# Optimization experiments

Measured on AMD Instinct MI355X. Metric: run time of the kernel, lower is better.

Reference implementation:

```python
import jax, jax.numpy as jnp
import numpy as np
import math

EMBED_DIM = 1024
NUM_HEADS = 16
D_K = EMBED_DIM // NUM_HEADS  # 64 qubits per head
BATCH, SEQ = 4, 2048


def setup_inputs() -> dict:
    key = jax.random.key(0)
    k_x, k_th, k_w, k_b = jax.random.split(key, 4)
    x = jax.random.normal(k_x, (BATCH, SEQ, EMBED_DIM), dtype=jnp.float32)
    # trainable RX angle per head per qubit (tq.RX has one param each)
    theta = jax.random.normal(k_th, (NUM_HEADS, D_K), dtype=jnp.float32)
    # out_linear
    lim = 1.0 / math.sqrt(EMBED_DIM)
    w_out = jax.random.uniform(k_w, (EMBED_DIM, EMBED_DIM), jnp.float32, -lim, lim)
    b_out = jax.random.uniform(k_b, (EMBED_DIM,), jnp.float32, -lim, lim)
    return {"x": x, "theta": theta, "w_out": w_out, "b_out": b_out}


def reference(x, theta, w_out, b_out):
    B, S, E = x.shape
    H, d_k = theta.shape
    # Quantum head: RX(x_i) then RX(theta_i) on |0>, measure PauliZ ->
    # <Z_i> = cos(x_i + theta_i). No entangling gates in the code path.
    ang = x.reshape(B, S, H, d_k) + theta  # broadcast [H,d_k]
    qkv = jnp.cos(ang).transpose(0, 2, 1, 3)  # [B,H,S,d_k]; Q == K == V
    scale = 1.0 / math.sqrt(d_k)
    scores = jnp.einsum('bhqd,bhkd->bhqk', qkv, qkv) * scale
    attn = jax.nn.softmax(scores, axis=-1)  # dropout is identity in eval
    out = jnp.einsum('bhqk,bhkd->bhqd', attn, qkv)
    out = out.transpose(0, 2, 1, 3).reshape(B, S, E)
    return out @ w_out.T + b_out
```

## Files before the change

kernel.cpp:

```cpp
#include <hip/hip_runtime.h>


#define B_  4
#define S_  2048
#define H_  16
#define D_  64
#define E_  1024
#define EXP2_SCALE 0.18033688011112043f

typedef unsigned short u16;
typedef unsigned int u32;
typedef __attribute__((ext_vector_type(8))) short short8;
typedef __attribute__((ext_vector_type(4))) float floatx4;

static __device__ __forceinline__ float bf2f(u16 v) {
    return __uint_as_float(((unsigned)v) << 16);
}
static __device__ __forceinline__ u16 f2bf(float f) {
    unsigned u = __float_as_uint(f);
    return (u16)((u + 0x7FFFu + ((u >> 16) & 1u)) >> 16);
}
static __device__ __forceinline__ u32 pack_bf16_trunc(float lo, float hi) {
    return __builtin_amdgcn_perm(__float_as_uint(hi), __float_as_uint(lo), 0x07060302u);
}
static __device__ __forceinline__ short8 scale8(short8 v) {
    short8 o;
#pragma unroll
    for (int i = 0; i < 8; i++)
        o[i] = (short)f2bf(bf2f((u16)v[i]) * EXP2_SCALE);
    return o;
}

#define KSWZ(r, c) ((((r)) << 6) + (((c) ^ ((((r)) & 7) << 3))))

__global__ __launch_bounds__(256) void prep_kernel(const float* __restrict__ x,
                                                   const float* __restrict__ theta,
                                                   const float* __restrict__ W,
                                                   u16* __restrict__ qkv,
                                                   u16* __restrict__ qkvT,
                                                   u16* __restrict__ Wb) {
    __shared__ __align__(16) u16 TQ[64][72];
    int blk = blockIdx.x;
    int tid = threadIdx.x;
    if (blk >= 2048) {
        int i = ((blk - 2048) * 256 + tid) * 4;
        float4 w = *(const float4*)(W + i);
        ushort4 o;
        o.x = f2bf(w.x); o.y = f2bf(w.y); o.z = f2bf(w.z); o.w = f2bf(w.w);
        *(ushort4*)(Wb + i) = o;
        return;
    }
    int stile = blk & 31;
    int bh    = blk >> 5;
    int b     = bh >> 4;
    int h     = bh & 15;
    int i     = tid >> 2;
    int d0    = (tid & 3) << 4;
    int s0    = stile << 6;
    int s     = s0 + i;

    const float* xp = x + ((size_t)(b * S_ + s)) * E_ + h * D_ + d0;
    const float* tp = theta + h * D_ + d0;

    u16 ov[16];
#pragma unroll
    for (int j = 0; j < 16; j += 4) {
        float4 xv = *(const float4*)(xp + j);
        float4 tv = *(const float4*)(tp + j);
        ov[j]     = f2bf(__cosf(xv.x + tv.x));
        ov[j + 1] = f2bf(__cosf(xv.y + tv.y));
        ov[j + 2] = f2bf(__cosf(xv.z + tv.z));
        ov[j + 3] = f2bf(__cosf(xv.w + tv.w));
    }

    u16* qp = qkv + ((size_t)bh * S_ + s) * D_ + d0;
    *(uint4*)qp       = *(uint4*)&ov[0];
    *(uint4*)(qp + 8) = *(uint4*)&ov[8];

#pragma unroll
    for (int j = 0; j < 16; j++) TQ[d0 + j][i] = ov[j];
    __syncthreads();

    int d  = tid >> 2;
    int j0 = (tid & 3) << 4;
    u16 tmp[16];
#pragma unroll
    for (int j = 0; j < 16; j++) tmp[j] = TQ[d][j0 + j];
    u16* qtp = qkvT + ((size_t)bh * D_ + d) * S_ + s0 + j0;
    *(uint4*)qtp       = *(uint4*)&tmp[0];
    *(uint4*)(qtp + 8) = *(uint4*)&tmp[8];
}

__global__ __launch_bounds__(256, 4) void attn_kernel(const u16* __restrict__ qkv,
                                                      const u16* __restrict__ qkvT,
                                                      u16* __restrict__ aout) {
    int blk0 = blockIdx.x;
    int blk  = (blk0 & 7) * 128 + (blk0 >> 3);
    int qt   = blk & 15;
    int bh   = blk >> 4;
    int b    = bh >> 4;
    int h    = bh & 15;
    int tid  = threadIdx.x;
    int wave = tid >> 6;
    int lane = tid & 63;
    int lq   = lane & 15;
    int lg   = lane >> 4;
    int r    = tid >> 2;
    int c0   = (tid & 3) << 4;

    __shared__ __align__(16) u16 Kt[64 * 64];
    __shared__ __align__(16) u16 Vt[64 * 64];
    __shared__ __align__(16) u16 Pb[4][32 * 64];

    const u16* base  = qkv  + (size_t)bh * S_ * D_;
    const u16* baseT = qkvT + (size_t)bh * D_ * S_;
    int s0 = qt * 128;

    short8 bq[2][2];
#pragma unroll
    for (int rf = 0; rf < 2; rf++) {
        const u16* qrow = base + (size_t)(s0 + wave * 32 + rf * 16 + lq) * D_ + lg * 8;
        bq[rf][0] = scale8(*(const short8*)qrow);
        bq[rf][1] = scale8(*(const short8*)(qrow + 32));
    }

    floatx4 oacc[2][4] = {{{0,0,0,0},{0,0,0,0},{0,0,0,0},{0,0,0,0}},
                          {{0,0,0,0},{0,0,0,0},{0,0,0,0},{0,0,0,0}}};
    float lsum[2] = {0.f, 0.f};

    {
        const u16* p = base + (size_t)r * D_ + c0;
        *(uint4*)&Kt[KSWZ(r, c0)]     = *(const uint4*)p;
        *(uint4*)&Kt[KSWZ(r, c0 + 8)] = *(const uint4*)(p + 8);
        const u16* p2 = baseT + (size_t)r * S_ + c0;
        *(uint4*)&Vt[KSWZ(r, c0)]     = *(const uint4*)p2;
        *(uint4*)&Vt[KSWZ(r, c0 + 8)] = *(const uint4*)(p2 + 8);
    }
    __syncthreads();

    for (int kt = 0; kt < S_ / 64; kt++) {
#pragma unroll
        for (int t = 0; t < 4; t++) {
            short8 a0 = *(short8*)&Kt[KSWZ(t * 16 + lq, lg * 8)];
            short8 a1 = *(short8*)&Kt[KSWZ(t * 16 + lq, 32 + lg * 8)];
            floatx4 sct[2];
#pragma unroll
            for (int rf = 0; rf < 2; rf++) {
                floatx4 acc = {0, 0, 0, 0};
                acc = __builtin_amdgcn_mfma_f32_16x16x32_bf16(a0, bq[rf][0], acc, 0, 0, 0);
                sct[rf] = __builtin_amdgcn_mfma_f32_16x16x32_bf16(a1, bq[rf][1], acc, 0, 0, 0);
            }
#pragma unroll
            for (int rf = 0; rf < 2; rf++) {
                float p0 = __builtin_amdgcn_exp2f(sct[rf][0]);
                float p1 = __builtin_amdgcn_exp2f(sct[rf][1]);
                float p2 = __builtin_amdgcn_exp2f(sct[rf][2]);
                float p3 = __builtin_amdgcn_exp2f(sct[rf][3]);
                lsum[rf] += (p0 + p1) + (p2 + p3);
                uint2 w;
                w.x = pack_bf16_trunc(p0, p1);
                w.y = pack_bf16_trunc(p2, p3);
                *(uint2*)&Pb[wave][KSWZ(rf * 16 + lq, t * 16 + lg * 4)] = w;
            }
        }

        asm volatile("s_waitcnt lgkmcnt(0)" ::: "memory");

        short8 bp[2][2];
#pragma unroll
        for (int rf = 0; rf < 2; rf++) {
            bp[rf][0] = *(short8*)&Pb[wave][KSWZ(rf * 16 + lq, lg * 8)];
            bp[rf][1] = *(short8*)&Pb[wave][KSWZ(rf * 16 + lq, 32 + lg * 8)];
        }
        __builtin_amdgcn_s_setprio(1);
#pragma unroll
        for (int t = 0; t < 4; t++) {
            short8 av0 = *(short8*)&Vt[KSWZ(t * 16 + lq, lg * 8)];
            short8 av1 = *(short8*)&Vt[KSWZ(t * 16 + lq, 32 + lg * 8)];
#pragma unroll
            for (int rf = 0; rf < 2; rf++) {
                oacc[rf][t] = __builtin_amdgcn_mfma_f32_16x16x32_bf16(av0, bp[rf][0], oacc[rf][t], 0, 0, 0);
                oacc[rf][t] = __builtin_amdgcn_mfma_f32_16x16x32_bf16(av1, bp[rf][1], oacc[rf][t], 0, 0, 0);
            }
        }
        __builtin_amdgcn_s_setprio(0);

        __syncthreads();
        if (kt < S_ / 64 - 1) {
            const u16* p = base + (size_t)((kt + 1) * 64 + r) * D_ + c0;
            uint4 k0 = *(const uint4*)p;
            uint4 k1 = *(const uint4*)(p + 8);
            const u16* p2 = baseT + (size_t)r * S_ + (kt + 1) * 64 + c0;
            uint4 v0 = *(const uint4*)p2;
            uint4 v1 = *(const uint4*)(p2 + 8);
            *(uint4*)&Kt[KSWZ(r, c0)]     = k0;
            *(uint4*)&Kt[KSWZ(r, c0 + 8)] = k1;
            *(uint4*)&Vt[KSWZ(r, c0)]     = v0;
            *(uint4*)&Vt[KSWZ(r, c0 + 8)] = v1;
        }
        __syncthreads();
    }

#pragma unroll
    for (int rf = 0; rf < 2; rf++) {
        lsum[rf] += __shfl_xor(lsum[rf], 16);
        lsum[rf] += __shfl_xor(lsum[rf], 32);
    }
#pragma unroll
    for (int rf = 0; rf < 2; rf++) {
        float inv = 1.0f / fmaxf(lsum[rf], 1e-20f);
        int srow = s0 + wave * 32 + rf * 16 + lq;
        u16* arow = aout + ((size_t)(b * S_ + srow)) * E_ + h * D_;
#pragma unroll
        for (int t = 0; t < 4; t++)
#pragma unroll
            for (int rr = 0; rr < 4; rr++)
                arow[t * 16 + lg * 4 + rr] = f2bf(oacc[rf][t][rr] * inv);
    }
}

__global__ __launch_bounds__(256) void proj_kernel(const u16* __restrict__ A,
                                                   const u16* __restrict__ Wb,
                                                   const float* __restrict__ bias,
                                                   float* __restrict__ out) {
    int m0   = blockIdx.x * 128;
    int n0   = blockIdx.y * 128;
    int tid  = threadIdx.x;
    int wave = tid >> 6;
    int wm   = wave >> 1;
    int wn   = wave & 1;
    int lane = tid & 63;
    int lq   = lane & 15;
    int lg   = lane >> 4;
    int r    = tid >> 1;
    int c0   = (tid & 1) * 32;

    __shared__ __align__(16) u16 As[128][72];
    __shared__ __align__(16) u16 Bs[128][72];

    floatx4 acc[4][4];
#pragma unroll
    for (int i = 0; i < 4; i++)
#pragma unroll
        for (int j = 0; j < 4; j++) acc[i][j] = (floatx4){0, 0, 0, 0};

    for (int kc = 0; kc < E_; kc += 64) {
        __syncthreads();
        const u16* pa = A + (size_t)(m0 + r) * E_ + kc + c0;
        const u16* pw = Wb + (size_t)(n0 + r) * E_ + kc + c0;
#pragma unroll
        for (int j = 0; j < 4; j++) {
            *(uint4*)&As[r][c0 + j * 8] = *(const uint4*)(pa + j * 8);
            *(uint4*)&Bs[r][c0 + j * 8] = *(const uint4*)(pw + j * 8);
        }
        __syncthreads();

#pragma unroll
        for (int c = 0; c < 2; c++) {
            short8 af[4], bf[4];
#pragma unroll
            for (int i = 0; i < 4; i++)
                af[i] = *(short8*)&As[wm * 64 + i * 16 + lq][c * 32 + lg * 8];
#pragma unroll
            for (int j = 0; j < 4; j++)
                bf[j] = *(short8*)&Bs[wn * 64 + j * 16 + lq][c * 32 + lg * 8];
#pragma unroll
            for (int i = 0; i < 4; i++)
#pragma unroll
                for (int j = 0; j < 4; j++)
                    acc[i][j] = __builtin_amdgcn_mfma_f32_16x16x32_bf16(af[i], bf[j], acc[i][j], 0, 0, 0);
        }
    }

#pragma unroll
    for (int j = 0; j < 4; j++) {
        int nidx = n0 + wn * 64 + j * 16 + lq;
        float bv = bias[nidx];
#pragma unroll
        for (int i = 0; i < 4; i++) {
#pragma unroll
            for (int rr = 0; rr < 4; rr++) {
                int row = m0 + wm * 64 + i * 16 + lg * 4 + rr;
                out[(size_t)row * E_ + nidx] = acc[i][j][rr] + bv;
            }
        }
    }
}

extern "C" void kernel_launch(void* const* d_in, const int* in_sizes, int n_in,
                              void* d_out, int out_size, void* d_ws, size_t ws_size,
                              hipStream_t stream) {
    const float* x     = (const float*)d_in[0];
    const float* theta = (const float*)d_in[1];
    const float* w_out = (const float*)d_in[2];
    const float* b_out = (const float*)d_in[3];
    float* out = (float*)d_out;

    char* ws = (char*)d_ws;
    const size_t QKV_BYTES = (size_t)B_ * H_ * S_ * D_ * sizeof(u16);
    u16* qkv  = (u16*)ws;
    u16* qkvT = (u16*)(ws + QKV_BYTES);
    u16* aout = (u16*)(ws + 2 * QKV_BYTES);
    u16* wbf_safe = (u16*)(ws + 3 * QKV_BYTES);

    prep_kernel<<<3072, 256, 0, stream>>>(x, theta, w_out, qkv, qkvT, wbf_safe);
    attn_kernel<<<(B_ * H_) * (S_ / 128), 256, 0, stream>>>(qkv, qkvT, aout);
    dim3 pg(B_ * S_ / 128, E_ / 128);
    proj_kernel<<<pg, 256, 0, stream>>>(aout, wbf_safe, b_out, out);
}
```

Baseline: 196.2 us.

## Keep softmax probabilities in registers and use 16x16x16 MFMA for PV

Drops the per-wave shared-memory staging of the P tile. Each lane's score output layout already matches the B operand of the 16x16x16 bf16 MFMA, so the probabilities feed the PV product straight from registers. This removes the LDS write, the wait and the read-back per key tile. In exchange it issues twice as many smaller MFMAs with narrower V reads, and it frees LDS, which may help occupancy.

New measurement: 204.2 us. 1.04x slower.

```diff
diff --git a/kernel.cpp b/kernel.cpp
--- a/kernel.cpp
+++ b/kernel.cpp
@@ -11,6 +11,7 @@
 typedef unsigned short u16;
 typedef unsigned int u32;
 typedef __attribute__((ext_vector_type(8))) short short8;
+typedef __attribute__((ext_vector_type(4))) short short4v;
 typedef __attribute__((ext_vector_type(4))) float floatx4;
 
 static __device__ __forceinline__ float bf2f(u16 v) {
@@ -29,6 +30,21 @@
     for (int i = 0; i < 8; i++)
         o[i] = (short)f2bf(bf2f((u16)v[i]) * EXP2_SCALE);
     return o;
+}
+
+#if defined(__has_builtin)
+#if __has_builtin(__builtin_amdgcn_mfma_f32_16x16x16bf16_1k)
+#define MFMA16_HAVE_BUILTIN 1
+#endif
+#endif
+static __device__ __forceinline__ floatx4 mfma16(short4v a, short4v b, floatx4 c) {
+#ifdef MFMA16_HAVE_BUILTIN
+    return __builtin_amdgcn_mfma_f32_16x16x16bf16_1k(a, b, c, 0, 0, 0);
+#else
+    floatx4 d = c;
+    asm("v_mfma_f32_16x16x16_bf16 %0, %1, %2, %0" : "+v"(d) : "v"(a), "v"(b));
+    return d;
+#endif
 }
 
 #define KSWZ(r, c) ((((r)) << 6) + (((c) ^ ((((r)) & 7) << 3))))
@@ -110,7 +126,6 @@
 
     __shared__ __align__(16) u16 Kt[64 * 64];
     __shared__ __align__(16) u16 Vt[64 * 64];
-    __shared__ __align__(16) u16 Pb[4][32 * 64];
 
     const u16* base  = qkv  + (size_t)bh * S_ * D_;
     const u16* baseT = qkvT + (size_t)bh * D_ * S_;
@@ -139,6 +154,7 @@
     __syncthreads();
 
     for (int kt = 0; kt < S_ / 64; kt++) {
+        short4v pb[2][4];
 #pragma unroll
         for (int t = 0; t < 4; t++) {
             short8 a0 = *(short8*)&Kt[KSWZ(t * 16 + lq, lg * 8)];
@@ -160,27 +176,18 @@
                 uint2 w;
                 w.x = pack_bf16_trunc(p0, p1);
                 w.y = pack_bf16_trunc(p2, p3);
-                *(uint2*)&Pb[wave][KSWZ(rf * 16 + lq, t * 16 + lg * 4)] = w;
+                pb[rf][t] = __builtin_bit_cast(short4v, w);
             }
         }
 
-        asm volatile("s_waitcnt lgkmcnt(0)" ::: "memory");
-
-        short8 bp[2][2];
-#pragma unroll
-        for (int rf = 0; rf < 2; rf++) {
-            bp[rf][0] = *(short8*)&Pb[wave][KSWZ(rf * 16 + lq, lg * 8)];
-            bp[rf][1] = *(short8*)&Pb[wave][KSWZ(rf * 16 + lq, 32 + lg * 8)];
-        }
         __builtin_amdgcn_s_setprio(1);
 #pragma unroll
-        for (int t = 0; t < 4; t++) {
-            short8 av0 = *(short8*)&Vt[KSWZ(t * 16 + lq, lg * 8)];
-            short8 av1 = *(short8*)&Vt[KSWZ(t * 16 + lq, 32 + lg * 8)];
-#pragma unroll
-            for (int rf = 0; rf < 2; rf++) {
-                oacc[rf][t] = __builtin_amdgcn_mfma_f32_16x16x32_bf16(av0, bp[rf][0], oacc[rf][t], 0, 0, 0);
-                oacc[rf][t] = __builtin_amdgcn_mfma_f32_16x16x32_bf16(av1, bp[rf][1], oacc[rf][t], 0, 0, 0);
+        for (int dt = 0; dt < 4; dt++) {
+#pragma unroll
+            for (int k4 = 0; k4 < 4; k4++) {
+                short4v av = *(short4v*)&Vt[KSWZ(dt * 16 + lq, k4 * 16 + lg * 4)];
+                oacc[0][dt] = mfma16(av, pb[0][k4], oacc[0][dt]);
+                oacc[1][dt] = mfma16(av, pb[1][k4], oacc[1][dt]);
             }
         }
         __builtin_amdgcn_s_setprio(0);
```

## Prefetch next K tile into registers and remap blocks in projection GEMM

Applied to the files above, without the earlier changes.

The projection GEMM now loads the next 64-wide K slice of A and W into registers while the MFMAs for the current slice run, then writes them to shared memory after a barrier. It also replaces the 2D grid with a 1D grid whose index is remapped so that neighbouring blocks in each group of eight share tiles, aiming for better L2 locality across XCDs. Launch bounds ask for two blocks per SM. This costs extra registers and may lower occupancy or cause spills.

Result: slower. 244.8 us (+24.7%).

```diff
diff --git a/kernel.cpp b/kernel.cpp
--- a/kernel.cpp
+++ b/kernel.cpp
@@ -219,12 +219,18 @@
     }
 }
 
-__global__ __launch_bounds__(256) void proj_kernel(const u16* __restrict__ A,
-                                                   const u16* __restrict__ Wb,
-                                                   const float* __restrict__ bias,
-                                                   float* __restrict__ out) {
-    int m0   = blockIdx.x * 128;
-    int n0   = blockIdx.y * 128;
+__global__ __launch_bounds__(256, 2) void proj_kernel(const u16* __restrict__ A,
+                                                      const u16* __restrict__ Wb,
+                                                      const float* __restrict__ bias,
+                                                      float* __restrict__ out) {
+    int b0 = blockIdx.x;
+    int xk = b0 & 7;
+    int rr_ = b0 >> 3;
+    int xb = xk * 8 + (rr_ & 7);
+    int yb = rr_ >> 3;
+    int m0 = xb * 128;
+    int n0 = yb * 128;
+
     int tid  = threadIdx.x;
     int wave = tid >> 6;
     int wm   = wave >> 1;
@@ -232,7 +238,7 @@
     int lane = tid & 63;
     int lq   = lane & 15;
     int lg   = lane >> 4;
-    int r    = tid >> 1;
+    int row  = tid >> 1;
     int c0   = (tid & 1) * 32;
 
     __shared__ __align__(16) u16 As[128][72];
@@ -244,16 +250,25 @@
 #pragma unroll
         for (int j = 0; j < 4; j++) acc[i][j] = (floatx4){0, 0, 0, 0};
 
+    const u16* pa0 = A  + (size_t)(m0 + row) * E_ + c0;
+    const u16* pw0 = Wb + (size_t)(n0 + row) * E_ + c0;
+
+#pragma unroll
+    for (int j = 0; j < 4; j++) {
+        *(uint4*)&As[row][c0 + j * 8] = *(const uint4*)(pa0 + j * 8);
+        *(uint4*)&Bs[row][c0 + j * 8] = *(const uint4*)(pw0 + j * 8);
+    }
+    __syncthreads();
+
     for (int kc = 0; kc < E_; kc += 64) {
-        __syncthreads();
-        const u16* pa = A + (size_t)(m0 + r) * E_ + kc + c0;
-        const u16* pw = Wb + (size_t)(n0 + r) * E_ + kc + c0;
-#pragma unroll
-        for (int j = 0; j < 4; j++) {
-            *(uint4*)&As[r][c0 + j * 8] = *(const uint4*)(pa + j * 8);
-            *(uint4*)&Bs[r][c0 + j * 8] = *(const uint4*)(pw + j * 8);
-        }
-        __syncthreads();
+        uint4 na[4], nb[4];
+        if (kc + 64 < E_) {
+#pragma unroll
+            for (int j = 0; j < 4; j++) {
+                na[j] = *(const uint4*)(pa0 + kc + 64 + j * 8);
+                nb[j] = *(const uint4*)(pw0 + kc + 64 + j * 8);
+            }
+        }
 
 #pragma unroll
         for (int c = 0; c < 2; c++) {
@@ -270,6 +285,16 @@
                 for (int j = 0; j < 4; j++)
                     acc[i][j] = __builtin_amdgcn_mfma_f32_16x16x32_bf16(af[i], bf[j], acc[i][j], 0, 0, 0);
         }
+
+        __syncthreads();
+        if (kc + 64 < E_) {
+#pragma unroll
+            for (int j = 0; j < 4; j++) {
+                *(uint4*)&As[row][c0 + j * 8] = na[j];
+                *(uint4*)&Bs[row][c0 + j * 8] = nb[j];
+            }
+        }
+        __syncthreads();
     }
 
 #pragma unroll
@@ -280,8 +305,8 @@
         for (int i = 0; i < 4; i++) {
 #pragma unroll
             for (int rr = 0; rr < 4; rr++) {
-                int row = m0 + wm * 64 + i * 16 + lg * 4 + rr;
-                out[(size_t)row * E_ + nidx] = acc[i][j][rr] + bv;
+                int orow = m0 + wm * 64 + i * 16 + lg * 4 + rr;
+                out[(size_t)orow * E_ + nidx] = acc[i][j][rr] + bv;
             }
         }
     }
@@ -305,6 +330,5 @@
 
     prep_kernel<<<3072, 256, 0, stream>>>(x, theta, w_out, qkv, qkvT, wbf_safe);
     attn_kernel<<<(B_ * H_) * (S_ / 128), 256, 0, stream>>>(qkv, qkvT, aout);
-    dim3 pg(B_ * S_ / 128, E_ / 128);
-    proj_kernel<<<pg, 256, 0, stream>>>(aout, wbf_safe, b_out, out);
-}
+    proj_kernel<<<512, 256, 0, stream>>>(aout, wbf_safe, b_out, out);
+}
```
